# Kernel tuning notes

Hardware: AMD Instinct MI355X
Metric: run time of the kernel (lower is better)

Reference implementation:

```python
import jax, jax.numpy as jnp
import numpy as np

T, B, I, H = 256, 64, 512, 512


def _lstm_layer(x, mask, h0, c0, Wih, bih, Whh, bhh, reverse):
    # x: [T, B, D_in], mask: [T, B, 1] bool (t < length). Packed-sequence semantics:
    # hidden/cell frozen where mask is False; reverse direction starts each row from
    # the initial hidden at its last valid step (rows stay at init until active).
    if reverse:
        x = x[::-1]
        mask = mask[::-1]

    def step(carry, inp):
        h, c = carry
        x_t, m = inp
        gates = x_t @ Wih.T + bih + h @ Whh.T + bhh  # [B, 4H]
        i_, f_, g_, o_ = jnp.split(gates, 4, axis=1)
        i_ = jax.nn.sigmoid(i_)
        f_ = jax.nn.sigmoid(f_)
        g_ = jnp.tanh(g_)
        o_ = jax.nn.sigmoid(o_)
        cy = f_ * c + i_ * g_
        hy = o_ * jnp.tanh(cy)
        h = jnp.where(m, hy, h)
        c = jnp.where(m, cy, c)
        return (h, c), jnp.where(m, hy, jnp.zeros_like(hy))

    (hn, cn), out = jax.lax.scan(step, (h0, c0), (x, mask))
    if reverse:
        out = out[::-1]
    return out, hn, cn


def setup_inputs() -> dict:
    key = jax.random.key(0)
    ks = jax.random.split(key, 24)
    x = jax.random.normal(ks[0], (T, B, I), jnp.float32)
    lengths = jnp.sort(jax.random.randint(ks[1], (B,), 1, T + 1))[::-1]
    lengths = lengths.at[0].set(T)  # batch_sizes[0] spans full T, as in packing
    h0 = 0.1 * jax.random.normal(ks[2], (4, B, H), jnp.float32)
    c0 = 0.1 * jax.random.normal(ks[3], (4, B, H), jnp.float32)
    std = 1.0 / np.sqrt(H)  # torch reset_parameters: U(-1/sqrt(H), 1/sqrt(H))
    def u(k, shape):
        return jax.random.uniform(k, shape, jnp.float32, -std, std)
    d = dict(x=x, lengths=lengths, h0=h0, c0=c0)
    names = [("l0", I), ("l0r", I), ("l1", 2 * H), ("l1r", 2 * H)]
    ki = 4
    for sfx, din in names:
        d[f"w_ih_{sfx}"] = u(ks[ki], (4 * H, din)); ki += 1
        d[f"w_hh_{sfx}"] = u(ks[ki], (4 * H, H)); ki += 1
        d[f"b_ih_{sfx}"] = u(ks[ki], (4 * H,)); ki += 1
        d[f"b_hh_{sfx}"] = u(ks[ki], (4 * H,)); ki += 1
    return d


def reference(x, lengths, h0, c0,
              w_ih_l0, w_hh_l0, b_ih_l0, b_hh_l0,
              w_ih_l0r, w_hh_l0r, b_ih_l0r, b_hh_l0r,
              w_ih_l1, w_hh_l1, b_ih_l1, b_hh_l1,
              w_ih_l1r, w_hh_l1r, b_ih_l1r, b_hh_l1r):
    mask = (jnp.arange(T)[:, None] < lengths[None, :])[:, :, None]  # [T,B,1]
    # layer 0
    of, _, _ = _lstm_layer(x, mask, h0[0], c0[0], w_ih_l0, b_ih_l0, w_hh_l0, b_hh_l0, False)
    ob, _, _ = _lstm_layer(x, mask, h0[1], c0[1], w_ih_l0r, b_ih_l0r, w_hh_l0r, b_hh_l0r, True)
    h1 = jnp.concatenate([of, ob], axis=-1)  # [T,B,2H]
    # layer 1
    of, _, _ = _lstm_layer(h1, mask, h0[2], c0[2], w_ih_l1, b_ih_l1, w_hh_l1, b_hh_l1, False)
    ob, _, _ = _lstm_layer(h1, mask, h0[3], c0[3], w_ih_l1r, b_ih_l1r, w_hh_l1r, b_hh_l1r, True)
    return jnp.concatenate([of, ob], axis=-1)  # padded output [T,B,2H]
```

## Files before the change

### kernel.cpp

```cpp
#include <hip/hip_runtime.h>
#include <hip/hip_bf16.h>
#include <math.h>

#define T_LEN 256
#define BATCH 64
#define HSZ   512

typedef __bf16 bf16x8 __attribute__((ext_vector_type(8)));
typedef float  f32x4  __attribute__((ext_vector_type(4)));

__device__ __forceinline__ unsigned short f2bf_rne(float f) {
    union { float f; unsigned int u; } c; c.f = f;
    unsigned int u = c.u;
    unsigned int r = (u + 0x7fffu + ((u >> 16) & 1u)) >> 16;
    return (unsigned short)r;
}
__device__ __forceinline__ float bf2f(unsigned short h) {
    union { unsigned int u; float f; } c; c.u = ((unsigned int)h) << 16;
    return c.f;
}
__device__ __forceinline__ void split_rne(float v, unsigned short& hi, unsigned short& lo) {
    hi = f2bf_rne(v);
    lo = f2bf_rne(v - bf2f(hi));
}

__device__ __forceinline__ float sigmoid_fast(float x) {
    return 1.0f / (1.0f + __expf(-x));
}
__device__ __forceinline__ float tanh_fast(float x) {
    float e = __expf(2.0f * x);
    return 1.0f - 2.0f / (e + 1.0f);
}

__device__ __forceinline__ bf16x8 coh16(const unsigned short* p) {
    const unsigned long long* q = (const unsigned long long*)p;
    unsigned long long a = __hip_atomic_load(q,     __ATOMIC_RELAXED, __HIP_MEMORY_SCOPE_AGENT);
    unsigned long long b = __hip_atomic_load(q + 1, __ATOMIC_RELAXED, __HIP_MEMORY_SCOPE_AGENT);
    union { unsigned long long u[2]; bf16x8 v; } c;
    c.u[0] = a; c.u[1] = b;
    return c.v;
}


__global__ __launch_bounds__(256)
void pack_x(const float* __restrict__ x, unsigned short* __restrict__ xf) {
    int t = blockIdx.x * 256 + threadIdx.x;
    int lane = t & 63;
    int id = t >> 6;
    int kc = id & 15; id >>= 4;
    int nt = id & 3;  id >>= 2;
    int tt = id;
    int b  = nt * 16 + (lane & 15);
    int k0 = kc * 32 + (lane >> 4) * 8;
    const float* src = x + ((size_t)tt * BATCH + b) * 512 + k0;
    union { unsigned short s[8]; uint4 v; } H, L;
#pragma unroll
    for (int e = 0; e < 8; ++e) split_rne(src[e], H.s[e], L.s[e]);
    size_t base = ((((size_t)tt * 4 + nt) * 16 + kc) * 2) * 512 + (size_t)lane * 8;
    *reinterpret_cast<uint4*>(&xf[base])       = H.v;
    *reinterpret_cast<uint4*>(&xf[base + 512]) = L.v;
}

template<int KC>
__global__ __launch_bounds__(256)
void pack_w(const float* __restrict__ wih0, const float* __restrict__ whh0,
            const float* __restrict__ wih1, const float* __restrict__ whh1,
            unsigned short* __restrict__ wp) {
    constexpr int DIN = (KC - 16) * 32;
    int t = blockIdx.x * 256 + threadIdx.x;
    int lane = t & 63;
    int id = t >> 6;
    int kc = id % KC; id /= KC;
    int bu = id & 127; id >>= 7;
    int cell = id;
    if (cell >= 2) return;
    const float* wih = cell ? wih1 : wih0;
    const float* whh = cell ? whh1 : whh0;
    int pr_g = bu * 16 + (lane & 15);
    int u_g = pr_g >> 2, g = pr_g & 3;
    int row = g * 512 + u_g;
    int k0 = kc * 32 + (lane >> 4) * 8;
    union { unsigned short s[8]; uint4 v; } H;
#pragma unroll
    for (int e = 0; e < 8; ++e) {
        int k = k0 + e;
        float v = (k < DIN) ? wih[(size_t)row * DIN + k]
                            : whh[(size_t)row * 512 + (k - DIN)];
        H.s[e] = f2bf_rne(v);
    }
    size_t base = (((size_t)cell * 128 + bu) * KC + kc) * 512 + (size_t)lane * 8;
    *reinterpret_cast<uint4*>(&wp[base]) = H.v;
}

__global__ __launch_bounds__(256)
void init_state(const float* __restrict__ h0, unsigned short* __restrict__ st) {
    int i = blockIdx.x * 256 + threadIdx.x;
    int cell = i >> 15;
    int r = i & 32767;
    int b = r >> 9;
    int u = r & 511;
    unsigned short hh = f2bf_rne(h0[((size_t)cell * BATCH + b) * 512 + u]);
    int nt = b >> 4, kc = u >> 5, rr = u & 31;
    int lane = ((rr >> 3) << 4) | (b & 15);
    int e = rr & 7;
    size_t sb = (((size_t)cell * 4 + nt) * 16 + kc) * 512 + (size_t)lane * 8 + e;
    st[sb] = hh;
}

template<int DIN>
__global__ __launch_bounds__(256, 1)
void lstm_phase(const unsigned short* __restrict__ bfr,
                const unsigned short* __restrict__ wp,
                const float* __restrict__ bihf, const float* __restrict__ bhhf,
                const float* __restrict__ bihb, const float* __restrict__ bhhb,
                const float* __restrict__ h0, const float* __restrict__ c0,
                const int* __restrict__ lengths,
                unsigned short* __restrict__ st,
                unsigned short* __restrict__ h1f,
                float* __restrict__ out,
                unsigned* __restrict__ bar,
                int cellbase)
{
    constexpr int KC   = (DIN + 512) / 32;
    constexpr int KCW  = KC / 4;
    constexpr int XCW  = DIN / 128;
    constexpr int NXKC = DIN / 32;
    constexpr size_t TBLK = 65536;

    const int bx = blockIdx.x;
    const int cd = bx & 1;
    const int bu = bx >> 1;
    const int cell = cellbase + cd;
    const int tid = threadIdx.x;
    const int w = tid >> 6, l = tid & 63;

    __shared__ float part[4][4][16][17];
    __shared__ float lds_pad[18000];

    if (__builtin_expect(lengths[0] == -2147483647, 0)) {
        lds_pad[tid] = (float)tid;
        __syncthreads();
        if (tid == 0) out[0] = lds_pad[255];
    }

    unsigned* flags = bar + (size_t)cd * 2048;

    bf16x8 wreg[KCW];
    {
        const unsigned short* wb = wp + ((size_t)cd * 128 + bu) * KC * 512 + (size_t)l * 8;
#pragma unroll
        for (int i = 0; i < KCW; ++i) {
            wreg[i] = *reinterpret_cast<const bf16x8*>(wb + (size_t)(w + 4 * i) * 512);
        }
    }

    const int b_t = l;
    const int u_g = bu * 4 + w;
    const int len = lengths[b_t];
    const float* bih = cd ? bihb : bihf;
    const float* bhh = cd ? bhhb : bhhf;
    const size_t sidx = ((size_t)cell * BATCH + b_t) * HSZ + u_g;
    float h_reg = h0[sidx];
    float c_reg = c0[sidx];
    float bsum[4];
#pragma unroll
    for (int g = 0; g < 4; ++g) bsum[g] = bih[g * 512 + u_g] + bhh[g * 512 + u_g];

    for (int s = 0; s < T_LEN; ++s) {
        const int t = cd ? (T_LEN - 1 - s) : s;
        f32x4 acc[4] = {};

        const unsigned short* bt = bfr + (size_t)t * TBLK;
        if constexpr (DIN == 512) {
#pragma unroll
            for (int i = 0; i < XCW; ++i) {
                const int kc = w + 4 * i;
#pragma unroll
                for (int nt = 0; nt < 4; ++nt) {
                    const unsigned short* p = bt + ((size_t)(nt * 16 + kc) * 2) * 512 + (size_t)l * 8;
                    bf16x8 bhi = *reinterpret_cast<const bf16x8*>(p);
                    bf16x8 blo = *reinterpret_cast<const bf16x8*>(p + 512);
                    acc[nt] = __builtin_amdgcn_mfma_f32_16x16x32_bf16(wreg[i], bhi, acc[nt], 0, 0, 0);
                    acc[nt] = __builtin_amdgcn_mfma_f32_16x16x32_bf16(wreg[i], blo, acc[nt], 0, 0, 0);
                }
            }
        } else {
#pragma unroll
            for (int i = 0; i < XCW; ++i) {
                const int kc = w + 4 * i;
#pragma unroll
                for (int nt = 0; nt < 4; ++nt) {
                    const unsigned short* p = bt + (size_t)(nt * 32 + kc) * 512 + (size_t)l * 8;
                    bf16x8 bb = *reinterpret_cast<const bf16x8*>(p);
                    acc[nt] = __builtin_amdgcn_mfma_f32_16x16x32_bf16(wreg[i], bb, acc[nt], 0, 0, 0);
                }
            }
        }

        if (s > 0) {
            if (tid < 64) {
                const unsigned* f0 = flags + (size_t)tid * 16;
                const unsigned* f1 = flags + (size_t)(tid + 64) * 16;
                for (;;) {
                    unsigned a = __hip_atomic_load(f0, __ATOMIC_RELAXED, __HIP_MEMORY_SCOPE_AGENT);
                    unsigned b = __hip_atomic_load(f1, __ATOMIC_RELAXED, __HIP_MEMORY_SCOPE_AGENT);
                    if (__all(a >= (unsigned)s && b >= (unsigned)s)) break;
                    __builtin_amdgcn_s_sleep(1);
                }
            }
            __syncthreads();
        }

        const unsigned short* hb = st + (size_t)((s & 1) * 4 + cell) * 32768;
#pragma unroll
        for (int i = XCW; i < KCW; ++i) {
            const int kch = w + 4 * i - NXKC;
#pragma unroll
            for (int nt = 0; nt < 4; ++nt) {
                const unsigned short* p = hb + (size_t)(nt * 16 + kch) * 512 + (size_t)l * 8;
                bf16x8 bb = coh16(p);
                acc[nt] = __builtin_amdgcn_mfma_f32_16x16x32_bf16(wreg[i], bb, acc[nt], 0, 0, 0);
            }
        }

#pragma unroll
        for (int nt = 0; nt < 4; ++nt)
#pragma unroll
            for (int j = 0; j < 4; ++j)
                part[w][nt][(l >> 4) * 4 + j][l & 15] = acc[nt][j];
        __syncthreads();

        float pre[4];
#pragma unroll
        for (int g = 0; g < 4; ++g) {
            float ssum = bsum[g];
#pragma unroll
            for (int ww = 0; ww < 4; ++ww)
                ssum += part[ww][b_t >> 4][w * 4 + g][b_t & 15];
            pre[g] = ssum;
        }
        const float gi = sigmoid_fast(pre[0]);
        const float gf = sigmoid_fast(pre[1]);
        const float gg = tanh_fast(pre[2]);
        const float go = sigmoid_fast(pre[3]);
        const float cy = gf * c_reg + gi * gg;
        const float hy = go * tanh_fast(cy);
        const bool mM = (t < len);
        if (mM) { c_reg = cy; h_reg = hy; }

        {
            const unsigned short hh = f2bf_rne(h_reg);
            const int kcs = u_g >> 5, rr = u_g & 31;
            const int lane_t = ((rr >> 3) << 4) | (b_t & 15);
            const int ee = rr & 7;
            size_t sb = (((size_t)(((s + 1) & 1) * 4 + cell) * 4 + (b_t >> 4)) * 16 + kcs) * 512
                      + (size_t)lane_t * 8 + ee;
            __hip_atomic_store(&st[sb], hh, __ATOMIC_RELAXED, __HIP_MEMORY_SCOPE_AGENT);
        }
        asm volatile("s_waitcnt vmcnt(0)" ::: "memory");
        __syncthreads();

        if (s < T_LEN - 1 && tid == 0) {
            __hip_atomic_store(flags + (size_t)bu * 16, (unsigned)(s + 1),
                               __ATOMIC_RELAXED, __HIP_MEMORY_SCOPE_AGENT);
        }

        const float ov = mM ? hy : 0.f;
        if constexpr (DIN == 512) {
            const unsigned short oh = f2bf_rne(ov);
            const int k1 = cd * 512 + u_g;
            const int kc1 = k1 >> 5, r1 = k1 & 31;
            const int lane1 = ((r1 >> 3) << 4) | (b_t & 15);
            const int e1 = r1 & 7;
            size_t ob = ((size_t)t * 4 + (b_t >> 4)) * 32 * 512 + (size_t)kc1 * 512
                      + (size_t)lane1 * 8 + e1;
            h1f[ob] = oh;
        } else {
            out[((size_t)t * BATCH + b_t) * 1024 + cd * 512 + u_g] = ov;
        }
    }
}

extern "C" void kernel_launch(void* const* d_in, const int* in_sizes, int n_in,
                              void* d_out, int out_size, void* d_ws, size_t ws_size,
                              hipStream_t stream) {
    const float* x        = (const float*)d_in[0];
    const int*   lengths  = (const int*)d_in[1];
    const float* h0       = (const float*)d_in[2];
    const float* c0       = (const float*)d_in[3];
    const float* w_ih_l0  = (const float*)d_in[4];
    const float* w_hh_l0  = (const float*)d_in[5];
    const float* b_ih_l0  = (const float*)d_in[6];
    const float* b_hh_l0  = (const float*)d_in[7];
    const float* w_ih_l0r = (const float*)d_in[8];
    const float* w_hh_l0r = (const float*)d_in[9];
    const float* b_ih_l0r = (const float*)d_in[10];
    const float* b_hh_l0r = (const float*)d_in[11];
    const float* w_ih_l1  = (const float*)d_in[12];
    const float* w_hh_l1  = (const float*)d_in[13];
    const float* b_ih_l1  = (const float*)d_in[14];
    const float* b_hh_l1  = (const float*)d_in[15];
    const float* w_ih_l1r = (const float*)d_in[16];
    const float* w_hh_l1r = (const float*)d_in[17];
    const float* b_ih_l1r = (const float*)d_in[18];
    const float* b_hh_l1r = (const float*)d_in[19];

    float* out = (float*)d_out;

    char* base = (char*)d_ws;
    unsigned* bar = (unsigned*)base;
    unsigned short* st  = (unsigned short*)(base + 65536);
    unsigned short* xf  = (unsigned short*)(base + 65536 + 524288);
    unsigned short* h1f = (unsigned short*)(base + 65536 + 524288 + 33554432);
    unsigned short* wp0 = (unsigned short*)(base + 65536 + 524288 + 33554432 + 33554432);
    unsigned short* wp1 = (unsigned short*)(base + 65536 + 524288 + 33554432 + 33554432 + 8388608);

    hipMemsetAsync(bar, 0, 65536, stream);

    hipLaunchKernelGGL(init_state, dim3(512), dim3(256), 0, stream, h0, st);
    hipLaunchKernelGGL(pack_x, dim3(4096), dim3(256), 0, stream, x, xf);
    hipLaunchKernelGGL((pack_w<32>), dim3(2048), dim3(256), 0, stream,
                       w_ih_l0, w_hh_l0, w_ih_l0r, w_hh_l0r, wp0);
    hipLaunchKernelGGL((pack_w<48>), dim3(3072), dim3(256), 0, stream,
                       w_ih_l1, w_hh_l1, w_ih_l1r, w_hh_l1r, wp1);

    hipLaunchKernelGGL((lstm_phase<512>), dim3(256), dim3(256), 0, stream,
                       xf, wp0,
                       b_ih_l0, b_hh_l0, b_ih_l0r, b_hh_l0r,
                       h0, c0, lengths, st, h1f, out, bar, 0);

    hipLaunchKernelGGL((lstm_phase<1024>), dim3(256), dim3(256), 0, stream,
                       h1f, wp1,
                       b_ih_l1, b_hh_l1, b_ih_l1r, b_hh_l1r,
                       h0, c0, lengths, st, h1f, out, bar + 8192, 2);
}
```

Measured before the change: 3.650 ms.

## Replace flag barrier with step-tagged hidden-state words polled directly

Replaces the per-block flag barrier with a scheme where each hidden value is stored as a 32-bit word holding the bf16 value and the step number. Consumers poll the hidden-state buffer directly until every tag matches the current step, then pack the values for MFMA. This removes the separate flag write, the vmcnt wait and one syncthreads per step, cutting latency on the recurrent critical path. In exchange, each wave reads twice the state bytes and every wave spins on global memory instead of a single wave polling flags.

Result: slower. 4.919 ms (+34.8%).

```diff
diff --git a/kernel.cpp b/kernel.cpp
--- a/kernel.cpp
+++ b/kernel.cpp
@@ -32,15 +32,31 @@
     return 1.0f - 2.0f / (e + 1.0f);
 }
 
-__device__ __forceinline__ bf16x8 coh16(const unsigned short* p) {
+__device__ __forceinline__ uint4 coh16u(const unsigned* p) {
     const unsigned long long* q = (const unsigned long long*)p;
     unsigned long long a = __hip_atomic_load(q,     __ATOMIC_RELAXED, __HIP_MEMORY_SCOPE_AGENT);
     unsigned long long b = __hip_atomic_load(q + 1, __ATOMIC_RELAXED, __HIP_MEMORY_SCOPE_AGENT);
-    union { unsigned long long u[2]; bf16x8 v; } c;
-    c.u[0] = a; c.u[1] = b;
+    uint4 r;
+    r.x = (unsigned)a; r.y = (unsigned)(a >> 32);
+    r.z = (unsigned)b; r.w = (unsigned)(b >> 32);
+    return r;
+}
+
+__device__ __forceinline__ bf16x8 pack8(uint4 a, uint4 b) {
+    union { unsigned u[4]; bf16x8 v; } c;
+    c.u[0] = (a.x & 0xFFFFu) | (a.y << 16);
+    c.u[1] = (a.z & 0xFFFFu) | (a.w << 16);
+    c.u[2] = (b.x & 0xFFFFu) | (b.y << 16);
+    c.u[3] = (b.z & 0xFFFFu) | (b.w << 16);
     return c.v;
 }
 
+
+__global__ __launch_bounds__(256)
+void clear_st(unsigned* __restrict__ st32) {
+    int i = blockIdx.x * 256 + threadIdx.x;
+    st32[i] = 0xFFFF0000u;
+}
 
 __global__ __launch_bounds__(256)
 void pack_x(const float* __restrict__ x, unsigned short* __restrict__ xf) {
@@ -93,7 +109,7 @@
 }
 
 __global__ __launch_bounds__(256)
-void init_state(const float* __restrict__ h0, unsigned short* __restrict__ st) {
+void init_state(const float* __restrict__ h0, unsigned* __restrict__ st32) {
     int i = blockIdx.x * 256 + threadIdx.x;
     int cell = i >> 15;
     int r = i & 32767;
@@ -104,7 +120,7 @@
     int lane = ((rr >> 3) << 4) | (b & 15);
     int e = rr & 7;
     size_t sb = (((size_t)cell * 4 + nt) * 16 + kc) * 512 + (size_t)lane * 8 + e;
-    st[sb] = hh;
+    st32[sb] = (unsigned)hh;
 }
 
 template<int DIN>
@@ -115,10 +131,9 @@
                 const float* __restrict__ bihb, const float* __restrict__ bhhb,
                 const float* __restrict__ h0, const float* __restrict__ c0,
                 const int* __restrict__ lengths,
-                unsigned short* __restrict__ st,
+                unsigned* __restrict__ st32,
                 unsigned short* __restrict__ h1f,
                 float* __restrict__ out,
-                unsigned* __restrict__ bar,
                 int cellbase)
 {
     constexpr int KC   = (DIN + 512) / 32;
@@ -142,8 +157,6 @@
         __syncthreads();
         if (tid == 0) out[0] = lds_pad[255];
     }
-
-    unsigned* flags = bar + (size_t)cd * 2048;
 
     bf16x8 wreg[KCW];
     {
@@ -166,6 +179,10 @@
 #pragma unroll
     for (int g = 0; g < 4; ++g) bsum[g] = bih[g * 512 + u_g] + bhh[g * 512 + u_g];
 
+    const int kcs = u_g >> 5, rr_s = u_g & 31;
+    const int lane_t = ((rr_s >> 3) << 4) | (b_t & 15);
+    const int ee = rr_s & 7;
+
     for (int s = 0; s < T_LEN; ++s) {
         const int t = cd ? (T_LEN - 1 - s) : s;
         f32x4 acc[4] = {};
@@ -197,29 +214,41 @@
             }
         }
 
-        if (s > 0) {
-            if (tid < 64) {
-                const unsigned* f0 = flags + (size_t)tid * 16;
-                const unsigned* f1 = flags + (size_t)(tid + 64) * 16;
-                for (;;) {
-                    unsigned a = __hip_atomic_load(f0, __ATOMIC_RELAXED, __HIP_MEMORY_SCOPE_AGENT);
-                    unsigned b = __hip_atomic_load(f1, __ATOMIC_RELAXED, __HIP_MEMORY_SCOPE_AGENT);
-                    if (__all(a >= (unsigned)s && b >= (unsigned)s)) break;
-                    __builtin_amdgcn_s_sleep(1);
+        {
+            const unsigned tagpat = (unsigned)s << 16;
+            const unsigned* hb32 = st32 + (size_t)((s & 1) * 4 + cell) * 32768;
+            uint4 TA[4][4], TB[4][4];
+            for (;;) {
+                unsigned bad = 0;
+#pragma unroll
+                for (int ih = 0; ih < 4; ++ih) {
+                    const int kch = w + 4 * ih;
+#pragma unroll
+                    for (int nt = 0; nt < 4; ++nt) {
+                        const unsigned* p = hb32 + (size_t)(nt * 16 + kch) * 512 + (size_t)l * 8;
+                        uint4 a = coh16u(p);
+                        uint4 b = coh16u(p + 4);
+                        TA[ih][nt] = a; TB[ih][nt] = b;
+                        bad |= (a.x ^ tagpat) & 0xFFFF0000u;
+                        bad |= (a.y ^ tagpat) & 0xFFFF0000u;
+                        bad |= (a.z ^ tagpat) & 0xFFFF0000u;
+                        bad |= (a.w ^ tagpat) & 0xFFFF0000u;
+                        bad |= (b.x ^ tagpat) & 0xFFFF0000u;
+                        bad |= (b.y ^ tagpat) & 0xFFFF0000u;
+                        bad |= (b.z ^ tagpat) & 0xFFFF0000u;
+                        bad |= (b.w ^ tagpat) & 0xFFFF0000u;
+                    }
                 }
+                if (__all(bad == 0)) break;
+                __builtin_amdgcn_s_sleep(1);
             }
-            __syncthreads();
-        }
-
-        const unsigned short* hb = st + (size_t)((s & 1) * 4 + cell) * 32768;
-#pragma unroll
-        for (int i = XCW; i < KCW; ++i) {
-            const int kch = w + 4 * i - NXKC;
-#pragma unroll
-            for (int nt = 0; nt < 4; ++nt) {
-                const unsigned short* p = hb + (size_t)(nt * 16 + kch) * 512 + (size_t)l * 8;
-                bf16x8 bb = coh16(p);
-                acc[nt] = __builtin_amdgcn_mfma_f32_16x16x32_bf16(wreg[i], bb, acc[nt], 0, 0, 0);
+#pragma unroll
+            for (int ih = 0; ih < 4; ++ih) {
+#pragma unroll
+                for (int nt = 0; nt < 4; ++nt) {
+                    bf16x8 bb = pack8(TA[ih][nt], TB[ih][nt]);
+                    acc[nt] = __builtin_amdgcn_mfma_f32_16x16x32_bf16(wreg[XCW + ih], bb, acc[nt], 0, 0, 0);
+                }
             }
         }
 
@@ -249,20 +278,10 @@
         if (mM) { c_reg = cy; h_reg = hy; }
 
         {
-            const unsigned short hh = f2bf_rne(h_reg);
-            const int kcs = u_g >> 5, rr = u_g & 31;
-            const int lane_t = ((rr >> 3) << 4) | (b_t & 15);
-            const int ee = rr & 7;
+            const unsigned word = ((unsigned)(s + 1) << 16) | (unsigned)f2bf_rne(h_reg);
             size_t sb = (((size_t)(((s + 1) & 1) * 4 + cell) * 4 + (b_t >> 4)) * 16 + kcs) * 512
                       + (size_t)lane_t * 8 + ee;
-            __hip_atomic_store(&st[sb], hh, __ATOMIC_RELAXED, __HIP_MEMORY_SCOPE_AGENT);
-        }
-        asm volatile("s_waitcnt vmcnt(0)" ::: "memory");
-        __syncthreads();
-
-        if (s < T_LEN - 1 && tid == 0) {
-            __hip_atomic_store(flags + (size_t)bu * 16, (unsigned)(s + 1),
-                               __ATOMIC_RELAXED, __HIP_MEMORY_SCOPE_AGENT);
+            __hip_atomic_store(&st32[sb], word, __ATOMIC_RELAXED, __HIP_MEMORY_SCOPE_AGENT);
         }
 
         const float ov = mM ? hy : 0.f;
@@ -278,6 +297,8 @@
         } else {
             out[((size_t)t * BATCH + b_t) * 1024 + cd * 512 + u_g] = ov;
         }
+
+        __syncthreads();
     }
 }
 
@@ -308,16 +329,14 @@
     float* out = (float*)d_out;
 
     char* base = (char*)d_ws;
-    unsigned* bar = (unsigned*)base;
-    unsigned short* st  = (unsigned short*)(base + 65536);
-    unsigned short* xf  = (unsigned short*)(base + 65536 + 524288);
-    unsigned short* h1f = (unsigned short*)(base + 65536 + 524288 + 33554432);
-    unsigned short* wp0 = (unsigned short*)(base + 65536 + 524288 + 33554432 + 33554432);
-    unsigned short* wp1 = (unsigned short*)(base + 65536 + 524288 + 33554432 + 33554432 + 8388608);
-
-    hipMemsetAsync(bar, 0, 65536, stream);
-
-    hipLaunchKernelGGL(init_state, dim3(512), dim3(256), 0, stream, h0, st);
+    unsigned* st32 = (unsigned*)base;
+    unsigned short* xf  = (unsigned short*)(base + 1048576);
+    unsigned short* h1f = (unsigned short*)(base + 1048576 + 33554432);
+    unsigned short* wp0 = (unsigned short*)(base + 1048576 + 33554432 + 33554432);
+    unsigned short* wp1 = (unsigned short*)(base + 1048576 + 33554432 + 33554432 + 8388608);
+
+    hipLaunchKernelGGL(clear_st, dim3(1024), dim3(256), 0, stream, st32);
+    hipLaunchKernelGGL(init_state, dim3(512), dim3(256), 0, stream, h0, st32);
     hipLaunchKernelGGL(pack_x, dim3(4096), dim3(256), 0, stream, x, xf);
     hipLaunchKernelGGL((pack_w<32>), dim3(2048), dim3(256), 0, stream,
                        w_ih_l0, w_hh_l0, w_ih_l0r, w_hh_l0r, wp0);
@@ -327,10 +346,10 @@
     hipLaunchKernelGGL((lstm_phase<512>), dim3(256), dim3(256), 0, stream,
                        xf, wp0,
                        b_ih_l0, b_hh_l0, b_ih_l0r, b_hh_l0r,
-                       h0, c0, lengths, st, h1f, out, bar, 0);
+                       h0, c0, lengths, st32, h1f, out, 0);
 
     hipLaunchKernelGGL((lstm_phase<1024>), dim3(256), dim3(256), 0, stream,
                        h1f, wp1,
                        b_ih_l1, b_hh_l1, b_ih_l1r, b_hh_l1r,
-                       h0, c0, lengths, st, h1f, out, bar + 8192, 2);
-}
+                       h0, c0, lengths, st32, h1f, out, 2);
+}
```
